# Kernel tuning notes

Hardware: AMD Instinct MI355X
Metric: run time of the kernel (lower is better)

The kernel has to match this reference:

```python
import jax, jax.numpy as jnp
import numpy as np

B, C, L, N, S = 32, 256, 512, 1024, 8  # batch, channels, seq_len, n_rois, output bins


def setup_inputs() -> dict:
    key = jax.random.key(0)
    k1, k2, k3 = jax.random.split(key, 3)
    sentences = jax.random.normal(k1, (B, C, L, 1), dtype=jnp.float32)
    rois = jnp.sort(jax.random.randint(k2, (N, 2), 0, L, dtype=jnp.int64), axis=1)
    # guarantee non-empty crop: x2 >= x1 + 1 (clamped into [0, L])
    x1 = jnp.minimum(rois[:, 0], L - 1)
    x2 = jnp.clip(rois[:, 1], x1 + 1, L)
    rois = jnp.stack([x1, x2], axis=1)
    roi_idx = jax.random.randint(k3, (N,), 0, B, dtype=jnp.int64)
    return {"sentences": sentences, "rois": rois, "roi_idx": roi_idx}


def reference(sentences, rois, roi_idx):
    # Gather per-ROI sentences; width dim is always sliced [0:1] -> drop it.
    x = sentences[roi_idx, :, :, 0]              # [N, C, L]
    x1 = rois[:, 0]                               # [N]
    x2 = rois[:, 1]                               # [N]
    lr = x2 - x1                                  # per-ROI crop length, >= 1
    pos = jnp.arange(L)[None, :]                  # [1, L]
    bins = []
    for j in range(S):  # fixed small loop over output bins
        # AdaptiveMaxPool bin j: [floor(j*lr/S), ceil((j+1)*lr/S)) offset by x1
        start = x1 + (j * lr) // S                # [N]
        end = x1 + ((j + 1) * lr + S - 1) // S    # [N]
        mask = (pos >= start[:, None]) & (pos < end[:, None])  # [N, L]
        masked = jnp.where(mask[:, None, :], x, -jnp.inf)       # [N, C, L]
        bins.append(masked.max(axis=-1))                         # [N, C]
    out = jnp.stack(bins, axis=-1)[..., None]     # [N, C, S, 1]
    return out
```

## Files before the change

kernel.cpp:

```cpp
#include <hip/hip_runtime.h>
#include <cfloat>

constexpr int Bc = 32;
constexpr int Cc = 256;
constexpr int Lc = 512;
constexpr int Nc = 1024;
constexpr int Sc = 8;

constexpr int CT      = 8;
constexpr int STRIDE  = 516;
constexpr int LSTRIDE = 132;

typedef float f4 __attribute__((ext_vector_type(4)));

__device__ __forceinline__ float chunkmax(f4 v, int lo, int hi, float m) {
    float a0 = (lo <= 0 && 0 < hi) ? v.x : -FLT_MAX;
    float a1 = (lo <= 1 && 1 < hi) ? v.y : -FLT_MAX;
    float a2 = (lo <= 2 && 2 < hi) ? v.z : -FLT_MAX;
    float a3 = (lo <= 3 && 3 < hi) ? v.w : -FLT_MAX;
    return fmaxf(fmaxf(m, fmaxf(a0, a1)), fmaxf(a2, a3));
}

__global__ __launch_bounds__(256) void roi_pool_pyr3(
    const float* __restrict__ sentences,
    const int*   __restrict__ rois,
    const int*   __restrict__ roi_idx,
    float*       __restrict__ out)
{
    __shared__ float rowbuf[CT * STRIDE];
    __shared__ float lvl1[CT * LSTRIDE];
    __shared__ int   list[Nc];
    __shared__ int   wcnt[16];

    const int bid  = blockIdx.x;
    const int b    = bid >> 5;
    const int c0   = (bid & 31) * CT;
    const int tid  = threadIdx.x;
    const int lane = tid & 63;
    const int w    = tid >> 6;

    int myidx[4], mypos[4];
    #pragma unroll
    for (int q = 0; q < 4; ++q) {
        const int i = q * 256 + tid;
        const int v = roi_idx[i];
        const unsigned long long mask = __ballot(v == b);
        mypos[q] = __popcll(mask & ((1ull << lane) - 1ull));
        myidx[q] = (v == b) ? i : -1;
        if (lane == 0) wcnt[q * 4 + w] = __popcll(mask);
    }

    {
        const f4* src = (const f4*)(sentences + ((size_t)b * Cc + c0) * Lc);
        #pragma unroll
        for (int i = 0; i < (CT * Lc / 4) / 256; ++i) {
            const int idx = tid + i * 256;
            const int r   = idx >> 7;
            const int q   = idx & 127;
            f4 v = src[r * (Lc / 4) + q];
            *(f4*)(rowbuf + r * STRIDE + 4 * q) = v;
            lvl1[r * LSTRIDE + q] = fmaxf(fmaxf(v.x, v.y), fmaxf(v.z, v.w));
        }
    }
    __syncthreads();

    int wb0 = 0, wb1 = 0, wb2 = 0, wb3 = 0, run = 0;
    #pragma unroll
    for (int t = 0; t < 16; ++t) {
        if (t == w)      wb0 = run;
        if (t == 4 + w)  wb1 = run;
        if (t == 8 + w)  wb2 = run;
        if (t == 12 + w) wb3 = run;
        run += wcnt[t];
    }
    const int m = run;

    if (myidx[0] >= 0) list[wb0 + mypos[0]] = myidx[0];
    if (myidx[1] >= 0) list[wb1 + mypos[1]] = myidx[1];
    if (myidx[2] >= 0) list[wb2 + mypos[2]] = myidx[2];
    if (myidx[3] >= 0) list[wb3 + mypos[3]] = myidx[3];
    __syncthreads();

    const int cl = lane >> 3;
    const int j  = lane & 7;
    const float* row = rowbuf + cl * STRIDE;
    const float* lv  = lvl1 + cl * LSTRIDE;

    for (int i = w; i < m; i += 4) {
        const int n  = list[i];
        const int x1 = rois[2 * n];
        const int x2 = rois[2 * n + 1];
        const int lr = x2 - x1;
        const int s  = x1 + ((j * lr) >> 3);
        const int e  = x1 + (((j + 1) * lr + Sc - 1) >> 3);

        const int qs = s >> 2;
        const int qe = e >> 2;

        f4 hv = *(const f4*)(row + 4 * qs);
        float mm = chunkmax(hv, s & 3, min(4, e - 4 * qs), -FLT_MAX);

        for (int q = qs + 1; q < qe; ++q)
            mm = fmaxf(mm, lv[q]);

        if ((e & 3) && qe > qs) {
            f4 tv = *(const f4*)(row + 4 * qe);
            mm = chunkmax(tv, 0, e & 3, mm);
        }

        out[(size_t)n * (Cc * Sc) + (c0 + cl) * Sc + j] = mm;
    }
}

extern "C" void kernel_launch(void* const* d_in, const int* in_sizes, int n_in,
                              void* d_out, int out_size, void* d_ws, size_t ws_size,
                              hipStream_t stream) {
    const float* sentences = (const float*)d_in[0];
    const int*   rois      = (const int*)d_in[1];
    const int*   roi_idx   = (const int*)d_in[2];
    float*       out       = (float*)d_out;

    roi_pool_pyr3<<<Bc * (Cc / CT), 256, 0, stream>>>(sentences, rois, roi_idx, out);
}
```

Measured before the change: 19.46 us.

## Split each tile across two blocks, drop level-1 max buffer, swizzle LDS rows

Launches twice as many blocks, each processing half of the ROI list for a (batch, channel-tile) pair, so every block reloads the same 16KB tile. Removes the precomputed 4-wide max level and scans raw float4 chunks directly, and uses an XOR-like rotation swizzle instead of padded strides. Shrinks the list to ushort and sets launch bounds for higher occupancy. The aims are more blocks in flight and lower LDS use, at the cost of duplicated global loads and more LDS reads per bin.

```diff
diff --git a/kernel.cpp b/kernel.cpp
--- a/kernel.cpp
+++ b/kernel.cpp
@@ -7,9 +7,7 @@
 constexpr int Nc = 1024;
 constexpr int Sc = 8;
 
-constexpr int CT      = 8;
-constexpr int STRIDE  = 516;
-constexpr int LSTRIDE = 132;
+constexpr int CT = 8;
 
 typedef float f4 __attribute__((ext_vector_type(4)));
 
@@ -21,45 +19,50 @@
     return fmaxf(fmaxf(m, fmaxf(a0, a1)), fmaxf(a2, a3));
 }
 
-__global__ __launch_bounds__(256) void roi_pool_pyr3(
+__device__ __forceinline__ int slot(int r, int q) {
+    return r * Lc + 4 * ((q + 4 * r) & 127);
+}
+
+__global__ __launch_bounds__(256, 8) void roi_pool_hiocc(
     const float* __restrict__ sentences,
     const int*   __restrict__ rois,
     const int*   __restrict__ roi_idx,
     float*       __restrict__ out)
 {
-    __shared__ float rowbuf[CT * STRIDE];
-    __shared__ float lvl1[CT * LSTRIDE];
-    __shared__ int   list[Nc];
-    __shared__ int   wcnt[16];
+    __shared__ float          rowbuf[CT * Lc];
+    __shared__ unsigned short list[Nc];
+    __shared__ int            wcnt[16];
 
     const int bid  = blockIdx.x;
-    const int b    = bid >> 5;
-    const int c0   = (bid & 31) * CT;
+    const int b    = bid >> 6;
+    const int ct   = (bid >> 1) & 31;
+    const int half = bid & 1;
+    const int c0   = ct * CT;
+
     const int tid  = threadIdx.x;
     const int lane = tid & 63;
     const int w    = tid >> 6;
 
-    int myidx[4], mypos[4];
+    int myn[4], mypos[4];
     #pragma unroll
     for (int q = 0; q < 4; ++q) {
         const int i = q * 256 + tid;
         const int v = roi_idx[i];
         const unsigned long long mask = __ballot(v == b);
         mypos[q] = __popcll(mask & ((1ull << lane) - 1ull));
-        myidx[q] = (v == b) ? i : -1;
+        myn[q]   = (v == b) ? i : -1;
         if (lane == 0) wcnt[q * 4 + w] = __popcll(mask);
     }
 
     {
         const f4* src = (const f4*)(sentences + ((size_t)b * Cc + c0) * Lc);
         #pragma unroll
-        for (int i = 0; i < (CT * Lc / 4) / 256; ++i) {
+        for (int i = 0; i < 4; ++i) {
             const int idx = tid + i * 256;
             const int r   = idx >> 7;
             const int q   = idx & 127;
-            f4 v = src[r * (Lc / 4) + q];
-            *(f4*)(rowbuf + r * STRIDE + 4 * q) = v;
-            lvl1[r * LSTRIDE + q] = fmaxf(fmaxf(v.x, v.y), fmaxf(v.z, v.w));
+            f4 v = src[r * 128 + q];
+            *(f4*)(rowbuf + slot(r, q)) = v;
         }
     }
     __syncthreads();
@@ -75,18 +78,16 @@
     }
     const int m = run;
 
-    if (myidx[0] >= 0) list[wb0 + mypos[0]] = myidx[0];
-    if (myidx[1] >= 0) list[wb1 + mypos[1]] = myidx[1];
-    if (myidx[2] >= 0) list[wb2 + mypos[2]] = myidx[2];
-    if (myidx[3] >= 0) list[wb3 + mypos[3]] = myidx[3];
+    if (myn[0] >= 0) list[wb0 + mypos[0]] = (unsigned short)myn[0];
+    if (myn[1] >= 0) list[wb1 + mypos[1]] = (unsigned short)myn[1];
+    if (myn[2] >= 0) list[wb2 + mypos[2]] = (unsigned short)myn[2];
+    if (myn[3] >= 0) list[wb3 + mypos[3]] = (unsigned short)myn[3];
     __syncthreads();
 
     const int cl = lane >> 3;
     const int j  = lane & 7;
-    const float* row = rowbuf + cl * STRIDE;
-    const float* lv  = lvl1 + cl * LSTRIDE;
 
-    for (int i = w; i < m; i += 4) {
+    for (int i = half + 2 * w; i < m; i += 8) {
         const int n  = list[i];
         const int x1 = rois[2 * n];
         const int x2 = rois[2 * n + 1];
@@ -95,17 +96,12 @@
         const int e  = x1 + (((j + 1) * lr + Sc - 1) >> 3);
 
         const int qs = s >> 2;
-        const int qe = e >> 2;
+        const int qe = (e - 1) >> 2;
 
-        f4 hv = *(const f4*)(row + 4 * qs);
-        float mm = chunkmax(hv, s & 3, min(4, e - 4 * qs), -FLT_MAX);
-
-        for (int q = qs + 1; q < qe; ++q)
-            mm = fmaxf(mm, lv[q]);
-
-        if ((e & 3) && qe > qs) {
-            f4 tv = *(const f4*)(row + 4 * qe);
-            mm = chunkmax(tv, 0, e & 3, mm);
+        float mm = -FLT_MAX;
+        for (int q = qs; q <= qe; ++q) {
+            f4 v = *(const f4*)(rowbuf + slot(cl, q));
+            mm = chunkmax(v, s - 4 * q, e - 4 * q, mm);
         }
 
         out[(size_t)n * (Cc * Sc) + (c0 + cl) * Sc + j] = mm;
@@ -120,5 +116,5 @@
     const int*   roi_idx   = (const int*)d_in[2];
     float*       out       = (float*)d_out;
 
-    roi_pool_pyr3<<<Bc * (Cc / CT), 256, 0, stream>>>(sentences, rois, roi_idx, out);
+    roi_pool_hiocc<<<Bc * (Cc / CT) * 2, 256, 0, stream>>>(sentences, rois, roi_idx, out);
 }
```

Result: slower. 27.38 us (+40.7%).

## Halve channel tile, pack ROI coords into list, process two ROIs per wave

Applied to the files above, without the earlier changes.

Reduces channels per block from 8 to 4, doubling the grid to 2048 blocks and shrinking shared memory, with launch bounds requesting 8 blocks per CU for higher occupancy. ROI bounds are loaded during list compaction and packed with the index into one int, removing dependent global loads of rois in the inner loop. Each wave now handles two ROIs at once (32 lanes per ROI), with a validity guard on the store. The cost is that roi_idx is scanned and the list compacted twice as often across blocks, and the padded strides change the LDS bank pattern.

```diff
diff --git a/kernel.cpp b/kernel.cpp
--- a/kernel.cpp
+++ b/kernel.cpp
@@ -7,9 +7,9 @@
 constexpr int Nc = 1024;
 constexpr int Sc = 8;
 
-constexpr int CT      = 8;
-constexpr int STRIDE  = 516;
-constexpr int LSTRIDE = 132;
+constexpr int CT      = 4;
+constexpr int STRIDE  = 524;
+constexpr int LSTRIDE = 133;
 
 typedef float f4 __attribute__((ext_vector_type(4)));
 
@@ -21,32 +21,38 @@
     return fmaxf(fmaxf(m, fmaxf(a0, a1)), fmaxf(a2, a3));
 }
 
-__global__ __launch_bounds__(256) void roi_pool_pyr3(
+__global__ __launch_bounds__(256, 8) void roi_pool_occ8(
     const float* __restrict__ sentences,
     const int*   __restrict__ rois,
     const int*   __restrict__ roi_idx,
     float*       __restrict__ out)
 {
-    __shared__ float rowbuf[CT * STRIDE];
+    __shared__ __align__(16) float rowbuf[CT * STRIDE];
     __shared__ float lvl1[CT * LSTRIDE];
     __shared__ int   list[Nc];
     __shared__ int   wcnt[16];
 
     const int bid  = blockIdx.x;
-    const int b    = bid >> 5;
-    const int c0   = (bid & 31) * CT;
+    const int b    = bid >> 6;
+    const int c0   = (bid & 63) * CT;
     const int tid  = threadIdx.x;
     const int lane = tid & 63;
     const int w    = tid >> 6;
 
-    int myidx[4], mypos[4];
+    int mypack[4], mypos[4];
     #pragma unroll
     for (int q = 0; q < 4; ++q) {
         const int i = q * 256 + tid;
         const int v = roi_idx[i];
         const unsigned long long mask = __ballot(v == b);
         mypos[q] = __popcll(mask & ((1ull << lane) - 1ull));
-        myidx[q] = (v == b) ? i : -1;
+        if (v == b) {
+            const int xx1 = rois[2 * i];
+            const int xx2 = rois[2 * i + 1];
+            mypack[q] = i | (xx1 << 10) | (xx2 << 20);
+        } else {
+            mypack[q] = -1;
+        }
         if (lane == 0) wcnt[q * 4 + w] = __popcll(mask);
     }
 
@@ -75,21 +81,26 @@
     }
     const int m = run;
 
-    if (myidx[0] >= 0) list[wb0 + mypos[0]] = myidx[0];
-    if (myidx[1] >= 0) list[wb1 + mypos[1]] = myidx[1];
-    if (myidx[2] >= 0) list[wb2 + mypos[2]] = myidx[2];
-    if (myidx[3] >= 0) list[wb3 + mypos[3]] = myidx[3];
+    if (mypack[0] >= 0) list[wb0 + mypos[0]] = mypack[0];
+    if (mypack[1] >= 0) list[wb1 + mypos[1]] = mypack[1];
+    if (mypack[2] >= 0) list[wb2 + mypos[2]] = mypack[2];
+    if (mypack[3] >= 0) list[wb3 + mypos[3]] = mypack[3];
     __syncthreads();
 
-    const int cl = lane >> 3;
+    const int ip = lane >> 5;
+    const int cl = (lane >> 3) & 3;
     const int j  = lane & 7;
     const float* row = rowbuf + cl * STRIDE;
     const float* lv  = lvl1 + cl * LSTRIDE;
 
-    for (int i = w; i < m; i += 4) {
-        const int n  = list[i];
-        const int x1 = rois[2 * n];
-        const int x2 = rois[2 * n + 1];
+    for (int i2 = 2 * w; i2 < m; i2 += 8) {
+        const int item  = i2 + ip;
+        const bool valid = item < m;
+        const int v  = list[valid ? item : i2];
+
+        const int n  = v & 1023;
+        const int x1 = (v >> 10) & 1023;
+        const int x2 = v >> 20;
         const int lr = x2 - x1;
         const int s  = x1 + ((j * lr) >> 3);
         const int e  = x1 + (((j + 1) * lr + Sc - 1) >> 3);
@@ -108,7 +119,8 @@
             mm = chunkmax(tv, 0, e & 3, mm);
         }
 
-        out[(size_t)n * (Cc * Sc) + (c0 + cl) * Sc + j] = mm;
+        if (valid)
+            out[(size_t)n * (Cc * Sc) + (c0 + cl) * Sc + j] = mm;
     }
 }
 
@@ -120,5 +132,5 @@
     const int*   roi_idx   = (const int*)d_in[2];
     float*       out       = (float*)d_out;
 
-    roi_pool_pyr3<<<Bc * (Cc / CT), 256, 0, stream>>>(sentences, rois, roi_idx, out);
+    roi_pool_occ8<<<Bc * (Cc / CT), 256, 0, stream>>>(sentences, rois, roi_idx, out);
 }
```

Result: slower. 20.17 us (+3.7%).
